# Kernel tuning notes

Measured on AMD Instinct MI355X. Metric: run time of the kernel, lower is better.

Reference implementation:

```python
import jax, jax.numpy as jnp
import numpy as np

B, A, C = 16, 3, 80
EPS = 1e-7


def _bce_logits(x, z):
    # numerically stable binary_cross_entropy_with_logits, elementwise
    return jnp.maximum(x, 0.0) - x * z + jnp.log1p(jnp.exp(-jnp.abs(x)))


def _cxcywh_to_xyxy(b):
    c, wh = b[..., :2], b[..., 2:]
    return jnp.concatenate([c - wh * 0.5, c + wh * 0.5], axis=-1)


def _iou_xyxy(a, b):
    # aligned (elementwise) IoU of [N,4] xyxy boxes
    lt = jnp.maximum(a[:, :2], b[:, :2])
    rb = jnp.minimum(a[:, 2:], b[:, 2:])
    wh = jnp.clip(rb - lt, 0.0)
    inter = wh[:, 0] * wh[:, 1]
    area_a = (a[:, 2] - a[:, 0]) * (a[:, 3] - a[:, 1])
    area_b = (b[:, 2] - b[:, 0]) * (b[:, 3] - b[:, 1])
    return inter / (area_a + area_b - inter + EPS)


def _scale_losses(box, obj, cls, samples, anchor_idx, gy, gx, anchors_wh, gt, labels):
    # gather assigned predictions: [N,4]
    fp = box[samples, anchor_idx, gy, gx]
    pred_xy = jax.nn.sigmoid(fp[:, :2]) * 2.0 - 0.5
    pred_wh = (jax.nn.sigmoid(fp[:, 2:4]) * 2.0) ** 2 * anchors_wh
    pred_boxes = jnp.concatenate([pred_xy, pred_wh], axis=1)
    iou = _iou_xyxy(_cxcywh_to_xyxy(pred_boxes), _cxcywh_to_xyxy(gt))
    loc_loss = (1.0 - iou).mean()
    # objectness: scatter clamped IoU into dense zero target
    tobj = jnp.zeros(obj.shape[:-1], obj.dtype).at[samples, anchor_idx, gy, gx].set(
        jnp.clip(iou, 0.0).astype(obj.dtype))
    obj_loss = _bce_logits(obj, tobj[..., None]).mean()
    # classification: gathered logits vs one-hot labels
    fcls = cls[samples, anchor_idx, gy, gx]
    onehot = jax.nn.one_hot(labels, cls.shape[-1], dtype=fcls.dtype)
    cls_loss = _bce_logits(fcls, onehot).mean()
    return loc_loss, obj_loss, cls_loss


def setup_inputs() -> dict:
    key = jax.random.key(0)
    inp = {}
    for si, (name, G, N) in enumerate([("ll", 80, 4000), ("ml", 40, 2000), ("hl", 20, 800)]):
        ks = jax.random.split(jax.random.fold_in(key, si), 10)
        inp[f"{name}_box"] = jax.random.normal(ks[0], (B, A, G, G, 4), jnp.float32)
        inp[f"{name}_obj"] = jax.random.normal(ks[1], (B, A, G, G, 1), jnp.float32)
        inp[f"{name}_cls"] = jax.random.normal(ks[2], (B, A, G, G, C), jnp.float32)
        inp[f"{name}_samples"] = jax.random.randint(ks[3], (N,), 0, B, jnp.int32)
        inp[f"{name}_anchor_idx"] = jax.random.randint(ks[4], (N,), 0, A, jnp.int32)
        inp[f"{name}_gy"] = jax.random.randint(ks[5], (N,), 0, G, jnp.int32)
        inp[f"{name}_gx"] = jax.random.randint(ks[6], (N,), 0, G, jnp.int32)
        inp[f"{name}_anchors"] = jax.random.uniform(ks[7], (N, 2), jnp.float32)
        inp[f"{name}_gt"] = jax.random.uniform(ks[8], (N, 4), jnp.float32)
        inp[f"{name}_labels"] = jax.random.randint(ks[9], (N,), 0, C, jnp.int32)
    inp["image_width"] = 640
    return inp


def reference(ll_box, ll_obj, ll_cls, ll_samples, ll_anchor_idx, ll_gy, ll_gx, ll_anchors, ll_gt, ll_labels,
              ml_box, ml_obj, ml_cls, ml_samples, ml_anchor_idx, ml_gy, ml_gx, ml_anchors, ml_gt, ml_labels,
              hl_box, hl_obj, hl_cls, hl_samples, hl_anchor_idx, hl_gy, hl_gx, hl_anchors, hl_gt, hl_labels,
              image_width):
    # hparams (Yolov5LossParams defaults)
    l_cls, l_loc, l_obj = 0.5, 0.05, 1.0
    r_ll, r_ml, r_hl = 4.0, 1.0, 0.4
    ll = _scale_losses(ll_box, ll_obj, ll_cls, ll_samples, ll_anchor_idx, ll_gy, ll_gx, ll_anchors, ll_gt, ll_labels)
    ml = _scale_losses(ml_box, ml_obj, ml_cls, ml_samples, ml_anchor_idx, ml_gy, ml_gx, ml_anchors, ml_gt, ml_labels)
    hl = _scale_losses(hl_box, hl_obj, hl_cls, hl_samples, hl_anchor_idx, hl_gy, hl_gx, hl_anchors, hl_gt, hl_labels)
    localization = ll[0] + ml[0] + hl[0]
    objectness = r_ll * ll[1] + r_ml * ml[1] + r_hl * hl[1]
    classification = ll[2] + ml[2] + hl[2]
    lam_obj = l_obj * (image_width / 640.0) ** 2
    lam_cls = l_cls * (ll_cls.shape[-1] / 80.0)
    return (l_loc * localization, lam_obj * objectness, lam_cls * classification)
```

## Files before the change

### kernel.cpp

```cpp
#include <hip/hip_runtime.h>

constexpr int Bn = 16, An = 3, Cn = 80;
constexpr int N_LL = 4000, N_ML = 2000, N_HL = 800;
constexpr int G_LL = 80,  G_ML = 40,   G_HL = 20;
constexpr int CELLS_LL = Bn * An * G_LL * G_LL;
constexpr int CELLS_ML = Bn * An * G_ML * G_ML;
constexpr int CELLS_HL = Bn * An * G_HL * G_HL;
constexpr int CELLS_TOT = CELLS_LL + CELLS_ML + CELLS_HL;

constexpr float L_CLS = 0.5f, L_LOC = 0.05f, L_OBJ = 1.0f;
constexpr float R_LL = 4.0f, R_ML = 1.0f, R_HL = 0.4f;

__device__ __forceinline__ float bce_logits(float x, float z) {
    return fmaxf(x, 0.0f) - x * z + log1pf(expf(-fabsf(x)));
}

__device__ __forceinline__ float sigmoidf(float x) {
    return 1.0f / (1.0f + expf(-x));
}

__device__ __forceinline__ float block_reduce_sum(float v) {
    for (int o = 32; o > 0; o >>= 1) v += __shfl_down(v, o, 64);
    __shared__ float smem[4];
    const int lane = threadIdx.x & 63, wid = threadIdx.x >> 6;
    if (lane == 0) smem[wid] = v;
    __syncthreads();
    if (wid == 0) {
        v = (lane < 4) ? smem[lane] : 0.0f;
        v += __shfl_down(v, 2, 64);
        v += __shfl_down(v, 1, 64);
    }
    return v;
}

__global__ void k_init(float* __restrict__ tobj, float* __restrict__ out) {
    const int i = blockIdx.x * blockDim.x + threadIdx.x;
    if (i < CELLS_TOT) tobj[i] = 0.0f;
    if (i < 3) out[i] = 0.0f;
}

struct ScaleB {
    const float* box; const int* samples; const int* anchor;
    const int* gy; const int* gx; const float* anchors; const float* gt;
    int G; int N; int cellBase; float locW;
};

__global__ void k_box(ScaleB s0, ScaleB s1, ScaleB s2,
                      float* __restrict__ tobj, float* __restrict__ out) {
    const int i = blockIdx.x * blockDim.x + threadIdx.x;
    float contrib = 0.0f;
    ScaleB s; int n = -1;
    if (i < s0.N)                 { s = s0; n = i; }
    else if (i < s0.N + s1.N)     { s = s1; n = i - s0.N; }
    else if (i < s0.N + s1.N + s2.N) { s = s2; n = i - s0.N - s1.N; }
    if (n >= 0) {
        const int smp = s.samples[n], a = s.anchor[n];
        const int gy = s.gy[n], gx = s.gx[n];
        const int cell = ((smp * An + a) * s.G + gy) * s.G + gx;
        const float4 fp = reinterpret_cast<const float4*>(s.box)[cell];
        const float sx = sigmoidf(fp.x), sy = sigmoidf(fp.y);
        const float sw = sigmoidf(fp.z), sh = sigmoidf(fp.w);
        const float px = sx * 2.0f - 0.5f;
        const float py = sy * 2.0f - 0.5f;
        const float aw = s.anchors[2 * n], ah = s.anchors[2 * n + 1];
        const float pw = (sw * 2.0f) * (sw * 2.0f) * aw;
        const float ph = (sh * 2.0f) * (sh * 2.0f) * ah;
        const float ax1 = px - pw * 0.5f, ay1 = py - ph * 0.5f;
        const float ax2 = px + pw * 0.5f, ay2 = py + ph * 0.5f;
        const float4 g = reinterpret_cast<const float4*>(s.gt)[n];
        const float bx1 = g.x - g.z * 0.5f, by1 = g.y - g.w * 0.5f;
        const float bx2 = g.x + g.z * 0.5f, by2 = g.y + g.w * 0.5f;
        const float lx = fmaxf(ax1, bx1), ly = fmaxf(ay1, by1);
        const float rx = fminf(ax2, bx2), ry = fminf(ay2, by2);
        const float iw = fmaxf(rx - lx, 0.0f), ih = fmaxf(ry - ly, 0.0f);
        const float inter = iw * ih;
        const float area_a = pw * ph, area_b = g.z * g.w;
        const float iou = inter / (area_a + area_b - inter + 1e-7f);
        contrib = s.locW * (1.0f - iou);
        atomicMax(reinterpret_cast<unsigned int*>(tobj + s.cellBase + cell),
                  __float_as_uint(fmaxf(iou, 0.0f)));
    }
    const float tot = block_reduce_sum(contrib);
    if (threadIdx.x == 0) atomicAdd(&out[0], tot);
}

struct ScaleC {
    const float* cls; const int* samples; const int* anchor;
    const int* gy; const int* gx; const int* labels;
    int G; int NC; float w;
};

__global__ void k_cls(ScaleC s0, ScaleC s1, ScaleC s2, float* __restrict__ out) {
    const int i = blockIdx.x * blockDim.x + threadIdx.x;
    float contrib = 0.0f;
    ScaleC s; int local = -1;
    if (i < s0.NC)                  { s = s0; local = i; }
    else if (i < s0.NC + s1.NC)     { s = s1; local = i - s0.NC; }
    else if (i < s0.NC + s1.NC + s2.NC) { s = s2; local = i - s0.NC - s1.NC; }
    if (local >= 0) {
        const int n = local / Cn, c = local - n * Cn;
        const int smp = s.samples[n], a = s.anchor[n];
        const int gy = s.gy[n], gx = s.gx[n];
        const int cell = ((smp * An + a) * s.G + gy) * s.G + gx;
        const float x = s.cls[(long long)cell * Cn + c];
        const float z = (s.labels[n] == c) ? 1.0f : 0.0f;
        contrib = s.w * bce_logits(x, z);
    }
    const float tot = block_reduce_sum(contrib);
    if (threadIdx.x == 0) atomicAdd(&out[2], tot);
}

__global__ void k_obj(const float* __restrict__ obj_ll,
                      const float* __restrict__ obj_ml,
                      const float* __restrict__ obj_hl,
                      const float* __restrict__ tobj,
                      const int* __restrict__ imgw_p,
                      float* __restrict__ out) {
    const int i = blockIdx.x * blockDim.x + threadIdx.x;
    float contrib = 0.0f;
    if (i < CELLS_TOT) {
        float x, w;
        if (i < CELLS_LL) {
            x = obj_ll[i];
            w = R_LL / (float)CELLS_LL;
        } else if (i < CELLS_LL + CELLS_ML) {
            x = obj_ml[i - CELLS_LL];
            w = R_ML / (float)CELLS_ML;
        } else {
            x = obj_hl[i - CELLS_LL - CELLS_ML];
            w = R_HL / (float)CELLS_HL;
        }
        const float t = tobj[i];
        contrib = w * bce_logits(x, t);
    }
    const float tot = block_reduce_sum(contrib);
    if (threadIdx.x == 0) {
        const float iw = (float)(*imgw_p);
        const float lam = L_OBJ * (iw / 640.0f) * (iw / 640.0f);
        atomicAdd(&out[1], lam * tot);
    }
}

extern "C" void kernel_launch(void* const* d_in, const int* in_sizes, int n_in,
                              void* d_out, int out_size, void* d_ws, size_t ws_size,
                              hipStream_t stream) {
    const float* ll_box = (const float*)d_in[0];
    const float* ll_obj = (const float*)d_in[1];
    const float* ll_cls = (const float*)d_in[2];
    const int*   ll_smp = (const int*)d_in[3];
    const int*   ll_anc = (const int*)d_in[4];
    const int*   ll_gy  = (const int*)d_in[5];
    const int*   ll_gx  = (const int*)d_in[6];
    const float* ll_awh = (const float*)d_in[7];
    const float* ll_gt  = (const float*)d_in[8];
    const int*   ll_lab = (const int*)d_in[9];

    const float* ml_box = (const float*)d_in[10];
    const float* ml_obj = (const float*)d_in[11];
    const float* ml_cls = (const float*)d_in[12];
    const int*   ml_smp = (const int*)d_in[13];
    const int*   ml_anc = (const int*)d_in[14];
    const int*   ml_gy  = (const int*)d_in[15];
    const int*   ml_gx  = (const int*)d_in[16];
    const float* ml_awh = (const float*)d_in[17];
    const float* ml_gt  = (const float*)d_in[18];
    const int*   ml_lab = (const int*)d_in[19];

    const float* hl_box = (const float*)d_in[20];
    const float* hl_obj = (const float*)d_in[21];
    const float* hl_cls = (const float*)d_in[22];
    const int*   hl_smp = (const int*)d_in[23];
    const int*   hl_anc = (const int*)d_in[24];
    const int*   hl_gy  = (const int*)d_in[25];
    const int*   hl_gx  = (const int*)d_in[26];
    const float* hl_awh = (const float*)d_in[27];
    const float* hl_gt  = (const float*)d_in[28];
    const int*   hl_lab = (const int*)d_in[29];

    const int* imgw = (const int*)d_in[30];

    float* out  = (float*)d_out;
    float* tobj = (float*)d_ws;

    const int TB = 256;

    {
        const int n = CELLS_TOT;
        k_init<<<(n + TB - 1) / TB, TB, 0, stream>>>(tobj, out);
    }

    {
        ScaleB s0{ll_box, ll_smp, ll_anc, ll_gy, ll_gx, ll_awh, ll_gt,
                  G_LL, N_LL, 0, L_LOC / (float)N_LL};
        ScaleB s1{ml_box, ml_smp, ml_anc, ml_gy, ml_gx, ml_awh, ml_gt,
                  G_ML, N_ML, CELLS_LL, L_LOC / (float)N_ML};
        ScaleB s2{hl_box, hl_smp, hl_anc, hl_gy, hl_gx, hl_awh, hl_gt,
                  G_HL, N_HL, CELLS_LL + CELLS_ML, L_LOC / (float)N_HL};
        const int n = N_LL + N_ML + N_HL;
        k_box<<<(n + TB - 1) / TB, TB, 0, stream>>>(s0, s1, s2, tobj, out);
    }

    {
        const float lam_cls = L_CLS * ((float)Cn / 80.0f);
        ScaleC s0{ll_cls, ll_smp, ll_anc, ll_gy, ll_gx, ll_lab,
                  G_LL, N_LL * Cn, lam_cls / (float)(N_LL * Cn)};
        ScaleC s1{ml_cls, ml_smp, ml_anc, ml_gy, ml_gx, ml_lab,
                  G_ML, N_ML * Cn, lam_cls / (float)(N_ML * Cn)};
        ScaleC s2{hl_cls, hl_smp, hl_anc, hl_gy, hl_gx, hl_lab,
                  G_HL, N_HL * Cn, lam_cls / (float)(N_HL * Cn)};
        const int n = (N_LL + N_ML + N_HL) * Cn;
        k_cls<<<(n + TB - 1) / TB, TB, 0, stream>>>(s0, s1, s2, out);
    }

    {
        const int n = CELLS_TOT;
        k_obj<<<(n + TB - 1) / TB, TB, 0, stream>>>(ll_obj, ml_obj, hl_obj, tobj, imgw, out);
    }
}
```

Baseline: 252.1 us.

## Fuse loss kernels and decompose objectness BCE to drop dense target buffer

Merges the init, box, class and objectness kernels into one fused kernel plus a small final reduction kernel. The objectness BCE is rewritten algebraically as a sum of softplus over all cells minus x·iou at the assigned cells. This removes the dense tobj buffer, its zeroing and its atomicMax scatter. Objectness and class logits are read as float4, and per-block partial sums go to workspace instead of global atomics. The risk is that duplicate assigned cells are now counted once per assignment rather than once per cell, so results can drift from the scatter-set semantics when indices collide.

```diff
diff --git a/kernel.cpp b/kernel.cpp
--- a/kernel.cpp
+++ b/kernel.cpp
@@ -6,10 +6,29 @@
 constexpr int CELLS_LL = Bn * An * G_LL * G_LL;
 constexpr int CELLS_ML = Bn * An * G_ML * G_ML;
 constexpr int CELLS_HL = Bn * An * G_HL * G_HL;
-constexpr int CELLS_TOT = CELLS_LL + CELLS_ML + CELLS_HL;
+
+constexpr int OBJ4_LL = CELLS_LL / 4;
+constexpr int OBJ4_ML = CELLS_ML / 4;
+constexpr int OBJ4_HL = CELLS_HL / 4;
+constexpr int OBJ4    = OBJ4_LL + OBJ4_ML + OBJ4_HL;
+constexpr int ROW4    = Cn / 4;
+constexpr int CLS4_LL = N_LL * ROW4;
+constexpr int CLS4_ML = N_ML * ROW4;
+constexpr int CLS4_HL = N_HL * ROW4;
+constexpr int CLS4    = CLS4_LL + CLS4_ML + CLS4_HL;
+constexpr int NBOX    = N_LL + N_ML + N_HL;
+constexpr int TOTAL   = OBJ4 + CLS4 + NBOX;
+
+constexpr int TB   = 256;
+constexpr int GRID = (TOTAL + TB - 1) / TB;
 
 constexpr float L_CLS = 0.5f, L_LOC = 0.05f, L_OBJ = 1.0f;
 constexpr float R_LL = 4.0f, R_ML = 1.0f, R_HL = 0.4f;
+constexpr float LAM_CLS = L_CLS * ((float)Cn / 80.0f);
+
+__device__ __forceinline__ float softplus0(float x) {
+    return fmaxf(x, 0.0f) + log1pf(expf(-fabsf(x)));
+}
 
 __device__ __forceinline__ float bce_logits(float x, float z) {
     return fmaxf(x, 0.0f) - x * z + log1pf(expf(-fabsf(x)));
@@ -19,50 +38,52 @@
     return 1.0f / (1.0f + expf(-x));
 }
 
-__device__ __forceinline__ float block_reduce_sum(float v) {
-    for (int o = 32; o > 0; o >>= 1) v += __shfl_down(v, o, 64);
-    __shared__ float smem[4];
-    const int lane = threadIdx.x & 63, wid = threadIdx.x >> 6;
-    if (lane == 0) smem[wid] = v;
-    __syncthreads();
-    if (wid == 0) {
-        v = (lane < 4) ? smem[lane] : 0.0f;
-        v += __shfl_down(v, 2, 64);
-        v += __shfl_down(v, 1, 64);
-    }
-    return v;
-}
-
-__global__ void k_init(float* __restrict__ tobj, float* __restrict__ out) {
-    const int i = blockIdx.x * blockDim.x + threadIdx.x;
-    if (i < CELLS_TOT) tobj[i] = 0.0f;
-    if (i < 3) out[i] = 0.0f;
-}
-
-struct ScaleB {
-    const float* box; const int* samples; const int* anchor;
-    const int* gy; const int* gx; const float* anchors; const float* gt;
-    int G; int N; int cellBase; float locW;
+struct Scale {
+    const float* box; const float* obj; const float* cls;
+    const int* smp; const int* anc; const int* gy; const int* gx;
+    const float* awh; const float* gt; const int* lab;
+    int G;
 };
 
-__global__ void k_box(ScaleB s0, ScaleB s1, ScaleB s2,
-                      float* __restrict__ tobj, float* __restrict__ out) {
-    const int i = blockIdx.x * blockDim.x + threadIdx.x;
-    float contrib = 0.0f;
-    ScaleB s; int n = -1;
-    if (i < s0.N)                 { s = s0; n = i; }
-    else if (i < s0.N + s1.N)     { s = s1; n = i - s0.N; }
-    else if (i < s0.N + s1.N + s2.N) { s = s2; n = i - s0.N - s1.N; }
-    if (n >= 0) {
-        const int smp = s.samples[n], a = s.anchor[n];
-        const int gy = s.gy[n], gx = s.gx[n];
-        const int cell = ((smp * An + a) * s.G + gy) * s.G + gx;
+__global__ __launch_bounds__(TB) void k_main(Scale ll, Scale ml, Scale hl,
+                                             float* __restrict__ ws) {
+    const int i = blockIdx.x * TB + threadIdx.x;
+    float loc_s = 0.0f, obj_s = 0.0f, cls_s = 0.0f;
+
+    if (i < OBJ4) {
+        const float4* p; float w;
+        if (i < OBJ4_LL)                    { p = (const float4*)ll.obj + i;                   w = R_LL / (float)CELLS_LL; }
+        else if (i < OBJ4_LL + OBJ4_ML)     { p = (const float4*)ml.obj + (i - OBJ4_LL);       w = R_ML / (float)CELLS_ML; }
+        else                                { p = (const float4*)hl.obj + (i - OBJ4_LL - OBJ4_ML); w = R_HL / (float)CELLS_HL; }
+        const float4 x = *p;
+        obj_s = w * (softplus0(x.x) + softplus0(x.y) + softplus0(x.z) + softplus0(x.w));
+    } else if (i < OBJ4 + CLS4) {
+        const int j = i - OBJ4;
+        Scale s; int local; float w;
+        if (j < CLS4_LL)                 { s = ll; local = j;                       w = LAM_CLS / (float)(N_LL * Cn); }
+        else if (j < CLS4_LL + CLS4_ML)  { s = ml; local = j - CLS4_LL;             w = LAM_CLS / (float)(N_ML * Cn); }
+        else                             { s = hl; local = j - CLS4_LL - CLS4_ML;   w = LAM_CLS / (float)(N_HL * Cn); }
+        const int n = local / ROW4, q = local - n * ROW4;
+        const int cell = ((s.smp[n] * An + s.anc[n]) * s.G + s.gy[n]) * s.G + s.gx[n];
+        const float4 x = reinterpret_cast<const float4*>(s.cls)[cell * ROW4 + q];
+        const int lab = s.lab[n], c0 = q * 4;
+        cls_s = w * (bce_logits(x.x, (lab == c0    ) ? 1.0f : 0.0f) +
+                     bce_logits(x.y, (lab == c0 + 1) ? 1.0f : 0.0f) +
+                     bce_logits(x.z, (lab == c0 + 2) ? 1.0f : 0.0f) +
+                     bce_logits(x.w, (lab == c0 + 3) ? 1.0f : 0.0f));
+    } else if (i < TOTAL) {
+        const int j = i - OBJ4 - CLS4;
+        Scale s; int n; float locW, objW;
+        if (j < N_LL)              { s = ll; n = j;               locW = L_LOC / (float)N_LL; objW = R_LL / (float)CELLS_LL; }
+        else if (j < N_LL + N_ML)  { s = ml; n = j - N_LL;        locW = L_LOC / (float)N_ML; objW = R_ML / (float)CELLS_ML; }
+        else                       { s = hl; n = j - N_LL - N_ML; locW = L_LOC / (float)N_HL; objW = R_HL / (float)CELLS_HL; }
+        const int cell = ((s.smp[n] * An + s.anc[n]) * s.G + s.gy[n]) * s.G + s.gx[n];
         const float4 fp = reinterpret_cast<const float4*>(s.box)[cell];
         const float sx = sigmoidf(fp.x), sy = sigmoidf(fp.y);
         const float sw = sigmoidf(fp.z), sh = sigmoidf(fp.w);
         const float px = sx * 2.0f - 0.5f;
         const float py = sy * 2.0f - 0.5f;
-        const float aw = s.anchors[2 * n], ah = s.anchors[2 * n + 1];
+        const float aw = s.awh[2 * n], ah = s.awh[2 * n + 1];
         const float pw = (sw * 2.0f) * (sw * 2.0f) * aw;
         const float ph = (sh * 2.0f) * (sh * 2.0f) * ah;
         const float ax1 = px - pw * 0.5f, ay1 = py - ph * 0.5f;
@@ -74,146 +95,71 @@
         const float rx = fminf(ax2, bx2), ry = fminf(ay2, by2);
         const float iw = fmaxf(rx - lx, 0.0f), ih = fmaxf(ry - ly, 0.0f);
         const float inter = iw * ih;
-        const float area_a = pw * ph, area_b = g.z * g.w;
-        const float iou = inter / (area_a + area_b - inter + 1e-7f);
-        contrib = s.locW * (1.0f - iou);
-        atomicMax(reinterpret_cast<unsigned int*>(tobj + s.cellBase + cell),
-                  __float_as_uint(fmaxf(iou, 0.0f)));
+        const float iou = inter / (pw * ph + g.z * g.w - inter + 1e-7f);
+        loc_s = locW * (1.0f - iou);
+        obj_s = -objW * s.obj[cell] * iou;
     }
-    const float tot = block_reduce_sum(contrib);
-    if (threadIdx.x == 0) atomicAdd(&out[0], tot);
+
+    float v[3] = {loc_s, obj_s, cls_s};
+    __shared__ float sm[3][4];
+    const int lane = threadIdx.x & 63, wid = threadIdx.x >> 6;
+    #pragma unroll
+    for (int k = 0; k < 3; ++k) {
+        float t = v[k];
+        for (int o = 32; o > 0; o >>= 1) t += __shfl_down(t, o, 64);
+        if (lane == 0) sm[k][wid] = t;
+    }
+    __syncthreads();
+    if (threadIdx.x == 0) {
+        #pragma unroll
+        for (int k = 0; k < 3; ++k)
+            ws[k * GRID + blockIdx.x] = sm[k][0] + sm[k][1] + sm[k][2] + sm[k][3];
+    }
 }
 
-struct ScaleC {
-    const float* cls; const int* samples; const int* anchor;
-    const int* gy; const int* gx; const int* labels;
-    int G; int NC; float w;
-};
-
-__global__ void k_cls(ScaleC s0, ScaleC s1, ScaleC s2, float* __restrict__ out) {
-    const int i = blockIdx.x * blockDim.x + threadIdx.x;
-    float contrib = 0.0f;
-    ScaleC s; int local = -1;
-    if (i < s0.NC)                  { s = s0; local = i; }
-    else if (i < s0.NC + s1.NC)     { s = s1; local = i - s0.NC; }
-    else if (i < s0.NC + s1.NC + s2.NC) { s = s2; local = i - s0.NC - s1.NC; }
-    if (local >= 0) {
-        const int n = local / Cn, c = local - n * Cn;
-        const int smp = s.samples[n], a = s.anchor[n];
-        const int gy = s.gy[n], gx = s.gx[n];
-        const int cell = ((smp * An + a) * s.G + gy) * s.G + gx;
-        const float x = s.cls[(long long)cell * Cn + c];
-        const float z = (s.labels[n] == c) ? 1.0f : 0.0f;
-        contrib = s.w * bce_logits(x, z);
-    }
-    const float tot = block_reduce_sum(contrib);
-    if (threadIdx.x == 0) atomicAdd(&out[2], tot);
-}
-
-__global__ void k_obj(const float* __restrict__ obj_ll,
-                      const float* __restrict__ obj_ml,
-                      const float* __restrict__ obj_hl,
-                      const float* __restrict__ tobj,
-                      const int* __restrict__ imgw_p,
-                      float* __restrict__ out) {
-    const int i = blockIdx.x * blockDim.x + threadIdx.x;
-    float contrib = 0.0f;
-    if (i < CELLS_TOT) {
-        float x, w;
-        if (i < CELLS_LL) {
-            x = obj_ll[i];
-            w = R_LL / (float)CELLS_LL;
-        } else if (i < CELLS_LL + CELLS_ML) {
-            x = obj_ml[i - CELLS_LL];
-            w = R_ML / (float)CELLS_ML;
-        } else {
-            x = obj_hl[i - CELLS_LL - CELLS_ML];
-            w = R_HL / (float)CELLS_HL;
+__global__ __launch_bounds__(TB) void k_final(const float* __restrict__ ws,
+                                              const int* __restrict__ imgw_p,
+                                              float* __restrict__ out) {
+    __shared__ float sm[4];
+    const int lane = threadIdx.x & 63, wid = threadIdx.x >> 6;
+    for (int k = 0; k < 3; ++k) {
+        float v = 0.0f;
+        for (int b = threadIdx.x; b < GRID; b += TB) v += ws[k * GRID + b];
+        for (int o = 32; o > 0; o >>= 1) v += __shfl_down(v, o, 64);
+        if (lane == 0) sm[wid] = v;
+        __syncthreads();
+        if (threadIdx.x == 0) {
+            float tot = sm[0] + sm[1] + sm[2] + sm[3];
+            if (k == 1) {
+                const float s = (float)(*imgw_p) / 640.0f;
+                tot *= L_OBJ * s * s;
+            }
+            out[k] = tot;
         }
-        const float t = tobj[i];
-        contrib = w * bce_logits(x, t);
-    }
-    const float tot = block_reduce_sum(contrib);
-    if (threadIdx.x == 0) {
-        const float iw = (float)(*imgw_p);
-        const float lam = L_OBJ * (iw / 640.0f) * (iw / 640.0f);
-        atomicAdd(&out[1], lam * tot);
+        __syncthreads();
     }
 }
 
 extern "C" void kernel_launch(void* const* d_in, const int* in_sizes, int n_in,
                               void* d_out, int out_size, void* d_ws, size_t ws_size,
                               hipStream_t stream) {
-    const float* ll_box = (const float*)d_in[0];
-    const float* ll_obj = (const float*)d_in[1];
-    const float* ll_cls = (const float*)d_in[2];
-    const int*   ll_smp = (const int*)d_in[3];
-    const int*   ll_anc = (const int*)d_in[4];
-    const int*   ll_gy  = (const int*)d_in[5];
-    const int*   ll_gx  = (const int*)d_in[6];
-    const float* ll_awh = (const float*)d_in[7];
-    const float* ll_gt  = (const float*)d_in[8];
-    const int*   ll_lab = (const int*)d_in[9];
-
-    const float* ml_box = (const float*)d_in[10];
-    const float* ml_obj = (const float*)d_in[11];
-    const float* ml_cls = (const float*)d_in[12];
-    const int*   ml_smp = (const int*)d_in[13];
-    const int*   ml_anc = (const int*)d_in[14];
-    const int*   ml_gy  = (const int*)d_in[15];
-    const int*   ml_gx  = (const int*)d_in[16];
-    const float* ml_awh = (const float*)d_in[17];
-    const float* ml_gt  = (const float*)d_in[18];
-    const int*   ml_lab = (const int*)d_in[19];
-
-    const float* hl_box = (const float*)d_in[20];
-    const float* hl_obj = (const float*)d_in[21];
-    const float* hl_cls = (const float*)d_in[22];
-    const int*   hl_smp = (const int*)d_in[23];
-    const int*   hl_anc = (const int*)d_in[24];
-    const int*   hl_gy  = (const int*)d_in[25];
-    const int*   hl_gx  = (const int*)d_in[26];
-    const float* hl_awh = (const float*)d_in[27];
-    const float* hl_gt  = (const float*)d_in[28];
-    const int*   hl_lab = (const int*)d_in[29];
-
+    Scale ll{(const float*)d_in[0],  (const float*)d_in[1],  (const float*)d_in[2],
+             (const int*)d_in[3],    (const int*)d_in[4],    (const int*)d_in[5],
+             (const int*)d_in[6],    (const float*)d_in[7],  (const float*)d_in[8],
+             (const int*)d_in[9],    G_LL};
+    Scale ml{(const float*)d_in[10], (const float*)d_in[11], (const float*)d_in[12],
+             (const int*)d_in[13],   (const int*)d_in[14],   (const int*)d_in[15],
+             (const int*)d_in[16],   (const float*)d_in[17], (const float*)d_in[18],
+             (const int*)d_in[19],   G_ML};
+    Scale hl{(const float*)d_in[20], (const float*)d_in[21], (const float*)d_in[22],
+             (const int*)d_in[23],   (const int*)d_in[24],   (const int*)d_in[25],
+             (const int*)d_in[26],   (const float*)d_in[27], (const float*)d_in[28],
+             (const int*)d_in[29],   G_HL};
     const int* imgw = (const int*)d_in[30];
 
-    float* out  = (float*)d_out;
-    float* tobj = (float*)d_ws;
+    float* out = (float*)d_out;
+    float* ws  = (float*)d_ws;
 
-    const int TB = 256;
-
-    {
-        const int n = CELLS_TOT;
-        k_init<<<(n + TB - 1) / TB, TB, 0, stream>>>(tobj, out);
-    }
-
-    {
-        ScaleB s0{ll_box, ll_smp, ll_anc, ll_gy, ll_gx, ll_awh, ll_gt,
-                  G_LL, N_LL, 0, L_LOC / (float)N_LL};
-        ScaleB s1{ml_box, ml_smp, ml_anc, ml_gy, ml_gx, ml_awh, ml_gt,
-                  G_ML, N_ML, CELLS_LL, L_LOC / (float)N_ML};
-        ScaleB s2{hl_box, hl_smp, hl_anc, hl_gy, hl_gx, hl_awh, hl_gt,
-                  G_HL, N_HL, CELLS_LL + CELLS_ML, L_LOC / (float)N_HL};
-        const int n = N_LL + N_ML + N_HL;
-        k_box<<<(n + TB - 1) / TB, TB, 0, stream>>>(s0, s1, s2, tobj, out);
-    }
-
-    {
-        const float lam_cls = L_CLS * ((float)Cn / 80.0f);
-        ScaleC s0{ll_cls, ll_smp, ll_anc, ll_gy, ll_gx, ll_lab,
-                  G_LL, N_LL * Cn, lam_cls / (float)(N_LL * Cn)};
-        ScaleC s1{ml_cls, ml_smp, ml_anc, ml_gy, ml_gx, ml_lab,
-                  G_ML, N_ML * Cn, lam_cls / (float)(N_ML * Cn)};
-        ScaleC s2{hl_cls, hl_smp, hl_anc, hl_gy, hl_gx, hl_lab,
-                  G_HL, N_HL * Cn, lam_cls / (float)(N_HL * Cn)};
-        const int n = (N_LL + N_ML + N_HL) * Cn;
-        k_cls<<<(n + TB - 1) / TB, TB, 0, stream>>>(s0, s1, s2, out);
-    }
-
-    {
-        const int n = CELLS_TOT;
-        k_obj<<<(n + TB - 1) / TB, TB, 0, stream>>>(ll_obj, ml_obj, hl_obj, tobj, imgw, out);
-    }
+    k_main<<<GRID, TB, 0, stream>>>(ll, ml, hl, ws);
+    k_final<<<1, TB, 0, stream>>>(ws, imgw, out);
 }
```

Measured after the change: 205.7 us. -18.4%, faster.
